# Kernel optimization log

Hardware: AMD Instinct MI355X
Metric: run time of the kernel (lower is better)

The kernel has to match this reference:

```python
import jax, jax.numpy as jnp
import numpy as np

IN_C = 256
OUT_C = 256
KQ_C = 256
HEADS = 8

def setup_inputs() -> dict:
    key = jax.random.key(0)
    kx, kq, kk, kv = jax.random.split(key, 4)
    N, T = 4, 2048
    x = jax.random.normal(kx, (N, IN_C, T), dtype=jnp.float32)
    # Conv1d(kernel_size=1, bias=False) weights: [out, in]
    s = 1.0 / np.sqrt(IN_C)
    Wq = jax.random.uniform(kq, (KQ_C, IN_C), dtype=jnp.float32, minval=-s, maxval=s)
    Wk = jax.random.uniform(kk, (KQ_C, IN_C), dtype=jnp.float32, minval=-s, maxval=s)
    Wv = jax.random.uniform(kv, (OUT_C, IN_C), dtype=jnp.float32, minval=-s, maxval=s)
    return {"x": x, "Wq": Wq, "Wk": Wk, "Wv": Wv}

def reference(x, Wq, Wk, Wv):
    N, C, T = x.shape
    H = HEADS
    dk = KQ_C // H   # head dim for q/k
    dv = OUT_C // H  # head dim for v
    # 1x1 conv == channel matmul: [N,C,T] -> [N,out,T]
    q = jnp.einsum('oc,nct->not', Wq, x).reshape(N, H, dk, T)
    k = jnp.einsum('oc,nct->not', Wk, x).reshape(N, H, dk, T)
    v = jnp.einsum('oc,nct->not', Wv, x).reshape(N, H, dv, T)
    # scores: [N,H,T,T] = q^T k, scaled
    scores = jnp.einsum('nhdt,nhds->nhts', q, k) / np.sqrt(dk).astype(jnp.float32)
    attn = jax.nn.softmax(scores, axis=-1)
    # out: [N,H,T,dv] -> [N,H,dv,T] -> [N,OUT_C,T]
    out = jnp.einsum('nhts,nhds->nhdt', attn, v)
    return out.reshape(N, OUT_C, T)
```

## Files before the change

kernel.cpp:

```cpp
#include <hip/hip_runtime.h>


typedef float f32x4 __attribute__((ext_vector_type(4)));
typedef short short8 __attribute__((ext_vector_type(8)));
typedef short short4v __attribute__((ext_vector_type(4)));

#define WS_Q 0u
#define WS_K (4u << 20)
#define WS_V (8u << 20)
#define WS_X (12u << 20)
#define WS_W (16u << 20)
#define WS_OP (20u << 20)

__device__ __forceinline__ unsigned short f2bf(float f) {
  unsigned int u = __builtin_bit_cast(unsigned int, f);
  u += 0x7FFFu + ((u >> 16) & 1u);
  return (unsigned short)(u >> 16);
}

__device__ __forceinline__ int pack_bf16rn(float a, float b) {
  unsigned int ua = __builtin_bit_cast(unsigned int, a) + 0x8000u;
  unsigned int ub = __builtin_bit_cast(unsigned int, b) + 0x8000u;
  return __builtin_amdgcn_perm(ub, ua, 0x07060302);
}

__global__ __launch_bounds__(256) void pack_kernel(
    const float* __restrict__ x, const float* __restrict__ Wq,
    const float* __restrict__ Wk, const float* __restrict__ Wv,
    unsigned short* __restrict__ ws) {
  const int tid = threadIdx.x;
  const int lane = tid & 63;
  const int wv = tid >> 6;
  const int lc = lane & 15, lq = lane >> 4;
  const int b = blockIdx.x;
  alignas(16) unsigned short tmp[8];
  if (b < 1024) {
    const int r = b * 4 + wv;
    const int kc = r & 7, tt = (r >> 3) & 127, n = r >> 10;
    const int t = tt * 16 + lc;
    const int c0 = kc * 32 + lq * 8;
    const float* src = x + (size_t)(n * 256 + c0) * 2048 + t;
#pragma unroll
    for (int j = 0; j < 8; ++j) tmp[j] = f2bf(src[(size_t)j * 2048]);
    unsigned short* dst = ws + (WS_X >> 1) + (size_t)r * 512 + lane * 8;
    *(int4*)dst = *(const int4*)tmp;
  } else {
    const int r = (b - 1024) * 4 + wv;
    const int kc = r & 7, ot = (r >> 3) & 15, wi = r >> 7;
    const float* W = (wi == 0) ? Wq : (wi == 1) ? Wk : Wv;
    const float scale = (wi == 0) ? 0.25503492f : 1.0f;
    const int o = ot * 16 + lc;
    const int c0 = kc * 32 + lq * 8;
    const float* src = W + o * 256 + c0;
#pragma unroll
    for (int j = 0; j < 8; ++j) tmp[j] = f2bf(src[j] * scale);
    unsigned short* dst = ws + (WS_W >> 1) + (size_t)r * 512 + lane * 8;
    *(int4*)dst = *(const int4*)tmp;
  }
}

__global__ __launch_bounds__(256) void proj_kernel(unsigned short* __restrict__ ws) {
  __shared__ unsigned short eps[4][2048];
  const int tid = threadIdx.x, lane = tid & 63, w = tid >> 6;
  const int lc = lane & 15, lq = lane >> 4;
  const int tt2 = blockIdx.x;
  const int n = blockIdx.y;
  const int wi = blockIdx.z;
  const unsigned short* Xb = ws + (WS_X >> 1);
  const unsigned short* Wb = ws + (WS_W >> 1);

  short8 af[2][8];
#pragma unroll
  for (int mt = 0; mt < 2; ++mt)
#pragma unroll
    for (int kc = 0; kc < 8; ++kc)
      af[mt][kc] = *(const short8*)(Xb + ((size_t)((n * 128 + tt2 * 2 + mt) * 8 + kc) * 512 + lane * 8));

  f32x4 acc[2][4];
#pragma unroll
  for (int mt = 0; mt < 2; ++mt)
#pragma unroll
    for (int nt = 0; nt < 4; ++nt) {
      f32x4 z = {0.f, 0.f, 0.f, 0.f};
      acc[mt][nt] = z;
    }

#pragma unroll
  for (int kc = 0; kc < 8; ++kc) {
    short8 bf[4];
#pragma unroll
    for (int nt = 0; nt < 4; ++nt)
      bf[nt] = *(const short8*)(Wb + ((size_t)((wi * 16 + w * 4 + nt) * 8 + kc) * 512 + lane * 8));
#pragma unroll
    for (int mt = 0; mt < 2; ++mt)
#pragma unroll
      for (int nt = 0; nt < 4; ++nt)
        acc[mt][nt] = __builtin_amdgcn_mfma_f32_16x16x32_bf16(af[mt][kc], bf[nt], acc[mt][nt], 0, 0, 0);
  }

  if (wi < 2) {
    unsigned short* ep = eps[w];
#pragma unroll
    for (int mt = 0; mt < 2; ++mt)
#pragma unroll
      for (int nt = 0; nt < 4; ++nt) {
        const int m2 = ((nt & 1) << 1) | (lc >> 3);
        const int base = ((mt * 2 + (nt >> 1)) << 9) + (m2 << 7) + (lq << 5) + (lc & 7);
#pragma unroll
        for (int r = 0; r < 4; ++r)
          ep[base + ((r ^ m2) << 3)] = f2bf(acc[mt][nt][r]);
      }
    const int swzl = lane ^ (lane >> 4);
    unsigned short* dst = ws + ((wi == 0) ? (WS_Q >> 1) : (WS_K >> 1));
#pragma unroll
    for (int rl = 0; rl < 4; ++rl) {
      int4 v = *(const int4*)(ep + (rl << 9) + swzl * 8);
      const int mt = rl >> 1, hh = rl & 1;
      const int nh = n * 8 + w * 2 + hh;
      const int ttg = tt2 * 2 + mt;
      *(int4*)(dst + ((size_t)(nh * 128 + ttg) * 64 + lane) * 8) = v;
    }
  } else {
    const int kb = tt2 >> 1, sbp = tt2 & 1;
#pragma unroll
    for (int nt = 0; nt < 4; ++nt) {
      const int nh = n * 8 + w * 2 + (nt >> 1);
      const int dt = nt & 1;
      alignas(16) unsigned short tmp[8];
#pragma unroll
      for (int mt = 0; mt < 2; ++mt)
#pragma unroll
        for (int r = 0; r < 4; ++r) tmp[mt * 4 + r] = f2bf(acc[mt][nt][r]);
      unsigned short* dstv = ws + (WS_V >> 1) +
          ((size_t)((((nh * 32 + kb) * 2 + dt) * 2 + sbp)) * 64 + lane) * 8;
      *(int4*)dstv = *(const int4*)tmp;
    }
  }
}

template <int KS>
__global__ __launch_bounds__(128, 3) void attn_kernel(
    const unsigned short* __restrict__ ws, float* __restrict__ out,
    unsigned short* __restrict__ opart, float* __restrict__ lpart) {
  const int tid = threadIdx.x;
  const int lane = tid & 63, wv = tid >> 6;
  const int lc = lane & 15, quad = lane >> 4;
  constexpr int CH = 32 * KS;
  const int c = blockIdx.x & (CH - 1);
  const int qx = blockIdx.x / CH;
  const int nh = c & 31;
  const int ks = c >> 5;
  const int qw = qx * 2 + wv;
  constexpr int NKB = 32 / KS;
  const int kb0 = ks * NKB;

  const unsigned short* Qw = ws + (WS_Q >> 1) + ((size_t)(nh * 128 + qw * 4)) * 512;
  const unsigned short* Kb = ws + (WS_K >> 1) + (size_t)nh * 65536;
  const unsigned short* Vb = ws + (WS_V >> 1) + (size_t)nh * 65536;

  short8 qf[4];
#pragma unroll
  for (int mt = 0; mt < 4; ++mt)
    qf[mt] = *(const short8*)(Qw + mt * 512 + lane * 8);

  f32x4 acc[4][2];
  f32x4 lsum_acc[4];
#pragma unroll
  for (int mt = 0; mt < 4; ++mt) {
    f32x4 z = {0.f, 0.f, 0.f, 0.f};
    acc[mt][0] = z;
    acc[mt][1] = z;
    lsum_acc[mt] = z;
  }
  const short4v onesf = {(short)0x3F80, (short)0x3F80, (short)0x3F80, (short)0x3F80};

  short8 kf[4], vv[4];
  {
    const unsigned short* kp = Kb + (size_t)kb0 * 2048 + lane * 8;
    const unsigned short* vp = Vb + (size_t)kb0 * 2048 + lane * 8;
#pragma unroll
    for (int u = 0; u < 4; ++u) kf[u] = *(const short8*)(kp + u * 512);
#pragma unroll
    for (int u = 0; u < 4; ++u) vv[u] = *(const short8*)(vp + u * 512);
  }

#pragma unroll 2
  for (int kb = kb0; kb < kb0 + NKB; ++kb) {
    const unsigned short* nkp = Kb + (size_t)(kb + 1) * 2048 + lane * 8;
    const unsigned short* nvp = Vb + (size_t)(kb + 1) * 2048 + lane * 8;
#pragma unroll
    for (int sb = 0; sb < 4; ++sb) {
      const short8 t0 = vv[(sb >> 1)];
      const short8 t1 = vv[2 + (sb >> 1)];
      short4v vf0, vf1;
      if (sb & 1) {
        vf0 = __builtin_shufflevector(t0, t0, 4, 5, 6, 7);
        vf1 = __builtin_shufflevector(t1, t1, 4, 5, 6, 7);
      } else {
        vf0 = __builtin_shufflevector(t0, t0, 0, 1, 2, 3);
        vf1 = __builtin_shufflevector(t1, t1, 0, 1, 2, 3);
      }
      f32x4 st[4];
#pragma unroll
      for (int mt = 0; mt < 4; ++mt) {
        f32x4 z = {0.f, 0.f, 0.f, 0.f};
        st[mt] = __builtin_amdgcn_mfma_f32_16x16x32_bf16(kf[sb], qf[mt], z, 0, 0, 0);
      }
      kf[sb] = *(const short8*)(nkp + sb * 512);
      if (sb == 1) {
        vv[0] = *(const short8*)(nvp + 0 * 512);
        vv[2] = *(const short8*)(nvp + 2 * 512);
      }
      if (sb == 3) {
        vv[1] = *(const short8*)(nvp + 1 * 512);
        vv[3] = *(const short8*)(nvp + 3 * 512);
      }
#pragma unroll
      for (int mt = 0; mt < 4; ++mt) {
        const float p0 = __builtin_amdgcn_exp2f(st[mt][0]);
        const float p1 = __builtin_amdgcn_exp2f(st[mt][1]);
        const float p2 = __builtin_amdgcn_exp2f(st[mt][2]);
        const float p3 = __builtin_amdgcn_exp2f(st[mt][3]);
        int2 pi;
        pi.x = pack_bf16rn(p0, p1);
        pi.y = pack_bf16rn(p2, p3);
        const short4v pf = __builtin_bit_cast(short4v, pi);
        lsum_acc[mt] = __builtin_amdgcn_mfma_f32_16x16x16bf16_1k(pf, onesf, lsum_acc[mt], 0, 0, 0);
        acc[mt][0] = __builtin_amdgcn_mfma_f32_16x16x16bf16_1k(pf, vf0, acc[mt][0], 0, 0, 0);
        acc[mt][1] = __builtin_amdgcn_mfma_f32_16x16x16bf16_1k(pf, vf1, acc[mt][1], 0, 0, 0);
      }
    }
  }

  if constexpr (KS == 1) {
    const int chbase = (nh >> 3) * 256 + (nh & 7) * 32;
#pragma unroll
    for (int mt = 0; mt < 4; ++mt) {
      f32x4 is;
#pragma unroll
      for (int r = 0; r < 4; ++r) is[r] = 1.0f / lsum_acc[mt][r];
      const int tb = qw * 64 + mt * 16 + quad * 4;
#pragma unroll
      for (int dt = 0; dt < 2; ++dt) {
        f32x4 ov;
#pragma unroll
        for (int r = 0; r < 4; ++r) ov[r] = acc[mt][dt][r] * is[r];
        *(f32x4*)(out + (size_t)(chbase + dt * 16 + lc) * 2048 + tb) = ov;
      }
    }
  } else {
    const size_t ob = (size_t)(ks * 32 + nh) * 32 * 2048;
#pragma unroll
    for (int mt = 0; mt < 4; ++mt) {
      const int tb = qw * 64 + mt * 16 + quad * 4;
#pragma unroll
      for (int dt = 0; dt < 2; ++dt) {
        int2 pi;
        pi.x = pack_bf16rn(acc[mt][dt][0], acc[mt][dt][1]);
        pi.y = pack_bf16rn(acc[mt][dt][2], acc[mt][dt][3]);
        *(int2*)(opart + ob + (size_t)(dt * 16 + lc) * 2048 + tb) = pi;
      }
      if (lc == 0)
        *(f32x4*)(lpart + (size_t)(ks * 32 + nh) * 2048 + qw * 64 + mt * 16 + quad * 4) = lsum_acc[mt];
    }
  }
}

template <int KS>
__global__ __launch_bounds__(256) void finalize_kernel(
    const unsigned short* __restrict__ opart, const float* __restrict__ lpart,
    float* __restrict__ out) {
  const int f = blockIdx.x * 256 + threadIdx.x;
  const int t4 = f & 511;
  const int c = f >> 9;
  const int n = c >> 8, ch = c & 255;
  const int nh = n * 8 + (ch >> 5), d = ch & 31;
  float o[4] = {0.f, 0.f, 0.f, 0.f};
  float l[4] = {0.f, 0.f, 0.f, 0.f};
#pragma unroll
  for (int ks = 0; ks < KS; ++ks) {
    const short4v ov = *(const short4v*)(opart + ((size_t)(ks * 32 + nh) * 32 + d) * 2048 + t4 * 4);
    const float4 lv = *(const float4*)(lpart + (size_t)(ks * 32 + nh) * 2048 + t4 * 4);
#pragma unroll
    for (int i = 0; i < 4; ++i) {
      const unsigned int u = ((unsigned int)(unsigned short)ov[i]) << 16;
      o[i] += __builtin_bit_cast(float, u);
    }
    l[0] += lv.x; l[1] += lv.y; l[2] += lv.z; l[3] += lv.w;
  }
  float4 r;
  r.x = o[0] / l[0]; r.y = o[1] / l[1]; r.z = o[2] / l[2]; r.w = o[3] / l[3];
  *(float4*)(out + (size_t)f * 4) = r;
}

extern "C" void kernel_launch(void* const* d_in, const int* in_sizes, int n_in,
                              void* d_out, int out_size, void* d_ws, size_t ws_size,
                              hipStream_t stream) {
  const float* x = (const float*)d_in[0];
  const float* Wq = (const float*)d_in[1];
  const float* Wk = (const float*)d_in[2];
  const float* Wv = (const float*)d_in[3];
  unsigned short* ws = (unsigned short*)d_ws;
  float* out = (float*)d_out;
  (void)in_sizes; (void)n_in; (void)out_size;

  pack_kernel<<<1120, 256, 0, stream>>>(x, Wq, Wk, Wv, ws);
  proj_kernel<<<dim3(64, 4, 3), 256, 0, stream>>>(ws);

  char* wsb = (char*)d_ws;
  unsigned short* opart = (unsigned short*)(wsb + WS_OP);
  if (ws_size >= ((size_t)41u << 20)) {
    float* lpart = (float*)(wsb + WS_OP + ((size_t)4 * 4u << 20));
    attn_kernel<4><<<2048, 128, 0, stream>>>(ws, out, opart, lpart);
    finalize_kernel<4><<<2048, 256, 0, stream>>>(opart, lpart, out);
  } else if (ws_size >= ((size_t)30u << 20)) {
    float* lpart = (float*)(wsb + WS_OP + ((size_t)2 * 4u << 20));
    attn_kernel<2><<<1024, 128, 0, stream>>>(ws, out, opart, lpart);
    finalize_kernel<2><<<2048, 256, 0, stream>>>(opart, lpart, out);
  } else {
    attn_kernel<1><<<512, 128, 0, stream>>>(ws, out, nullptr, nullptr);
  }
}
```

Baseline: 113.0 us.

## Replace split-K attention and finalize pass with smaller query tiles per wave

Removes the key-split path that wrote bf16 partial outputs and row sums and then ran a separate finalize kernel. Each wave now handles 32 queries instead of 64 and runs the full key loop, so there are 1024 blocks without any partial-result traffic. The intent is to drop the extra kernel launch and the workspace round-trip. In exchange, each loaded K/V fragment is reused across half as many queries, which doubles total K/V load traffic relative to the query work.

```diff
diff --git a/kernel.cpp b/kernel.cpp
--- a/kernel.cpp
+++ b/kernel.cpp
@@ -10,7 +10,6 @@
 #define WS_V (8u << 20)
 #define WS_X (12u << 20)
 #define WS_W (16u << 20)
-#define WS_OP (20u << 20)
 
 __device__ __forceinline__ unsigned short f2bf(float f) {
   unsigned int u = __builtin_bit_cast(unsigned int, f);
@@ -138,35 +137,28 @@
   }
 }
 
-template <int KS>
-__global__ __launch_bounds__(128, 3) void attn_kernel(
-    const unsigned short* __restrict__ ws, float* __restrict__ out,
-    unsigned short* __restrict__ opart, float* __restrict__ lpart) {
+__global__ __launch_bounds__(128, 2) void attn_kernel(
+    const unsigned short* __restrict__ ws, float* __restrict__ out) {
   const int tid = threadIdx.x;
   const int lane = tid & 63, wv = tid >> 6;
   const int lc = lane & 15, quad = lane >> 4;
-  constexpr int CH = 32 * KS;
-  const int c = blockIdx.x & (CH - 1);
-  const int qx = blockIdx.x / CH;
-  const int nh = c & 31;
-  const int ks = c >> 5;
+  const int c = blockIdx.x & 31;
+  const int qx = blockIdx.x >> 5;
+  const int nh = c;
   const int qw = qx * 2 + wv;
-  constexpr int NKB = 32 / KS;
-  const int kb0 = ks * NKB;
-
-  const unsigned short* Qw = ws + (WS_Q >> 1) + ((size_t)(nh * 128 + qw * 4)) * 512;
+
+  const unsigned short* Qw = ws + (WS_Q >> 1) + ((size_t)(nh * 128 + qw * 2)) * 512;
   const unsigned short* Kb = ws + (WS_K >> 1) + (size_t)nh * 65536;
   const unsigned short* Vb = ws + (WS_V >> 1) + (size_t)nh * 65536;
 
-  short8 qf[4];
-#pragma unroll
-  for (int mt = 0; mt < 4; ++mt)
-    qf[mt] = *(const short8*)(Qw + mt * 512 + lane * 8);
-
-  f32x4 acc[4][2];
-  f32x4 lsum_acc[4];
-#pragma unroll
-  for (int mt = 0; mt < 4; ++mt) {
+  short8 qf[2];
+  qf[0] = *(const short8*)(Qw + lane * 8);
+  qf[1] = *(const short8*)(Qw + 512 + lane * 8);
+
+  f32x4 acc[2][2];
+  f32x4 lsum_acc[2];
+#pragma unroll
+  for (int mt = 0; mt < 2; ++mt) {
     f32x4 z = {0.f, 0.f, 0.f, 0.f};
     acc[mt][0] = z;
     acc[mt][1] = z;
@@ -176,8 +168,8 @@
 
   short8 kf[4], vv[4];
   {
-    const unsigned short* kp = Kb + (size_t)kb0 * 2048 + lane * 8;
-    const unsigned short* vp = Vb + (size_t)kb0 * 2048 + lane * 8;
+    const unsigned short* kp = Kb + lane * 8;
+    const unsigned short* vp = Vb + lane * 8;
 #pragma unroll
     for (int u = 0; u < 4; ++u) kf[u] = *(const short8*)(kp + u * 512);
 #pragma unroll
@@ -185,7 +177,7 @@
   }
 
 #pragma unroll 2
-  for (int kb = kb0; kb < kb0 + NKB; ++kb) {
+  for (int kb = 0; kb < 32; ++kb) {
     const unsigned short* nkp = Kb + (size_t)(kb + 1) * 2048 + lane * 8;
     const unsigned short* nvp = Vb + (size_t)(kb + 1) * 2048 + lane * 8;
 #pragma unroll
@@ -200,9 +192,9 @@
         vf0 = __builtin_shufflevector(t0, t0, 0, 1, 2, 3);
         vf1 = __builtin_shufflevector(t1, t1, 0, 1, 2, 3);
       }
-      f32x4 st[4];
-#pragma unroll
-      for (int mt = 0; mt < 4; ++mt) {
+      f32x4 st[2];
+#pragma unroll
+      for (int mt = 0; mt < 2; ++mt) {
         f32x4 z = {0.f, 0.f, 0.f, 0.f};
         st[mt] = __builtin_amdgcn_mfma_f32_16x16x32_bf16(kf[sb], qf[mt], z, 0, 0, 0);
       }
@@ -216,7 +208,7 @@
         vv[3] = *(const short8*)(nvp + 3 * 512);
       }
 #pragma unroll
-      for (int mt = 0; mt < 4; ++mt) {
+      for (int mt = 0; mt < 2; ++mt) {
         const float p0 = __builtin_amdgcn_exp2f(st[mt][0]);
         const float p1 = __builtin_amdgcn_exp2f(st[mt][1]);
         const float p2 = __builtin_amdgcn_exp2f(st[mt][2]);
@@ -232,65 +224,21 @@
     }
   }
 
-  if constexpr (KS == 1) {
-    const int chbase = (nh >> 3) * 256 + (nh & 7) * 32;
-#pragma unroll
-    for (int mt = 0; mt < 4; ++mt) {
-      f32x4 is;
-#pragma unroll
-      for (int r = 0; r < 4; ++r) is[r] = 1.0f / lsum_acc[mt][r];
-      const int tb = qw * 64 + mt * 16 + quad * 4;
-#pragma unroll
-      for (int dt = 0; dt < 2; ++dt) {
-        f32x4 ov;
-#pragma unroll
-        for (int r = 0; r < 4; ++r) ov[r] = acc[mt][dt][r] * is[r];
-        *(f32x4*)(out + (size_t)(chbase + dt * 16 + lc) * 2048 + tb) = ov;
-      }
-    }
-  } else {
-    const size_t ob = (size_t)(ks * 32 + nh) * 32 * 2048;
-#pragma unroll
-    for (int mt = 0; mt < 4; ++mt) {
-      const int tb = qw * 64 + mt * 16 + quad * 4;
-#pragma unroll
-      for (int dt = 0; dt < 2; ++dt) {
-        int2 pi;
-        pi.x = pack_bf16rn(acc[mt][dt][0], acc[mt][dt][1]);
-        pi.y = pack_bf16rn(acc[mt][dt][2], acc[mt][dt][3]);
-        *(int2*)(opart + ob + (size_t)(dt * 16 + lc) * 2048 + tb) = pi;
-      }
-      if (lc == 0)
-        *(f32x4*)(lpart + (size_t)(ks * 32 + nh) * 2048 + qw * 64 + mt * 16 + quad * 4) = lsum_acc[mt];
-    }
-  }
-}
-
-template <int KS>
-__global__ __launch_bounds__(256) void finalize_kernel(
-    const unsigned short* __restrict__ opart, const float* __restrict__ lpart,
-    float* __restrict__ out) {
-  const int f = blockIdx.x * 256 + threadIdx.x;
-  const int t4 = f & 511;
-  const int c = f >> 9;
-  const int n = c >> 8, ch = c & 255;
-  const int nh = n * 8 + (ch >> 5), d = ch & 31;
-  float o[4] = {0.f, 0.f, 0.f, 0.f};
-  float l[4] = {0.f, 0.f, 0.f, 0.f};
-#pragma unroll
-  for (int ks = 0; ks < KS; ++ks) {
-    const short4v ov = *(const short4v*)(opart + ((size_t)(ks * 32 + nh) * 32 + d) * 2048 + t4 * 4);
-    const float4 lv = *(const float4*)(lpart + (size_t)(ks * 32 + nh) * 2048 + t4 * 4);
-#pragma unroll
-    for (int i = 0; i < 4; ++i) {
-      const unsigned int u = ((unsigned int)(unsigned short)ov[i]) << 16;
-      o[i] += __builtin_bit_cast(float, u);
-    }
-    l[0] += lv.x; l[1] += lv.y; l[2] += lv.z; l[3] += lv.w;
-  }
-  float4 r;
-  r.x = o[0] / l[0]; r.y = o[1] / l[1]; r.z = o[2] / l[2]; r.w = o[3] / l[3];
-  *(float4*)(out + (size_t)f * 4) = r;
+  const int chbase = (nh >> 3) * 256 + (nh & 7) * 32;
+#pragma unroll
+  for (int mt = 0; mt < 2; ++mt) {
+    f32x4 is;
+#pragma unroll
+    for (int r = 0; r < 4; ++r) is[r] = 1.0f / lsum_acc[mt][r];
+    const int tb = qw * 32 + mt * 16 + quad * 4;
+#pragma unroll
+    for (int dt = 0; dt < 2; ++dt) {
+      f32x4 ov;
+#pragma unroll
+      for (int r = 0; r < 4; ++r) ov[r] = acc[mt][dt][r] * is[r];
+      *(f32x4*)(out + (size_t)(chbase + dt * 16 + lc) * 2048 + tb) = ov;
+    }
+  }
 }
 
 extern "C" void kernel_launch(void* const* d_in, const int* in_sizes, int n_in,
@@ -302,22 +250,9 @@
   const float* Wv = (const float*)d_in[3];
   unsigned short* ws = (unsigned short*)d_ws;
   float* out = (float*)d_out;
-  (void)in_sizes; (void)n_in; (void)out_size;
+  (void)in_sizes; (void)n_in; (void)out_size; (void)ws_size;
 
   pack_kernel<<<1120, 256, 0, stream>>>(x, Wq, Wk, Wv, ws);
   proj_kernel<<<dim3(64, 4, 3), 256, 0, stream>>>(ws);
-
-  char* wsb = (char*)d_ws;
-  unsigned short* opart = (unsigned short*)(wsb + WS_OP);
-  if (ws_size >= ((size_t)41u << 20)) {
-    float* lpart = (float*)(wsb + WS_OP + ((size_t)4 * 4u << 20));
-    attn_kernel<4><<<2048, 128, 0, stream>>>(ws, out, opart, lpart);
-    finalize_kernel<4><<<2048, 256, 0, stream>>>(opart, lpart, out);
-  } else if (ws_size >= ((size_t)30u << 20)) {
-    float* lpart = (float*)(wsb + WS_OP + ((size_t)2 * 4u << 20));
-    attn_kernel<2><<<1024, 128, 0, stream>>>(ws, out, opart, lpart);
-    finalize_kernel<2><<<2048, 256, 0, stream>>>(opart, lpart, out);
-  } else {
-    attn_kernel<1><<<512, 128, 0, stream>>>(ws, out, nullptr, nullptr);
-  }
-}
+  attn_kernel<<<1024, 128, 0, stream>>>(ws, out);
+}
```

Result: no change. 112.0 us (-0.8%).
